# Performance work log

Hardware: AMD Instinct MI355X
Metric: run time of the kernel (lower is better)

## Reference

```python
import jax, jax.numpy as jnp
import numpy as np

B, N, INDIM, OUTDIM = 32, 128, 32, 64


def setup_inputs() -> dict:
    key = jax.random.key(0)
    k1, k2, k3, k4, k5, k6 = jax.random.split(key, 6)
    X = jax.random.normal(k1, (B, N, N, INDIM), dtype=jnp.float32)
    # variable subgraph sizes (irregular masking), at least 1 node per graph
    n_nodes = jnp.clip(jax.random.randint(k2, (B,), 0, N), 1, N).astype(jnp.int64)
    # MLP params (Linear + ReLU tail activation) for lin1 and lin2
    s = 1.0 / np.sqrt(INDIM)
    W1 = jax.random.uniform(k3, (INDIM, OUTDIM), jnp.float32, -s, s)
    b1 = jax.random.uniform(k4, (OUTDIM,), jnp.float32, -s, s)
    W2 = jax.random.uniform(k5, (INDIM, OUTDIM), jnp.float32, -s, s)
    b2 = jax.random.uniform(k6, (OUTDIM,), jnp.float32, -s, s)
    return {"X": X, "W1": W1, "b1": b1, "W2": W2, "b2": b2, "n_nodes": n_nodes}


def reference(X, W1, b1, W2, b2, n_nodes):
    # pairwise mask [B,N,N,1] from per-graph node counts (MaskedTensor mode 'DD')
    nm = jnp.arange(N)[None, :] < n_nodes[:, None]          # [B,N] node mask
    mask = (nm[:, :, None] & nm[:, None, :])[..., None].astype(X.dtype)  # [B,N,N,1]
    # tuplewiseapply of lin1 / lin2 (Linear + ReLU), zero-fill masked tuples
    X1 = jax.nn.relu(jnp.einsum('bijd,de->bije', X, W1) + b1) * mask  # [B,N,N,OUTDIM]
    X2 = jax.nn.relu(jnp.einsum('bijd,de->bije', X, W2) + b2) * mask
    # Op2FWL (aggr='sum'): per-channel batched matmul over node dim k
    out = jnp.einsum('bike,bkje->bije', X1, X2) * mask
    return out
```

## Files before the change

kernel.cpp:

```cpp
#include <hip/hip_runtime.h>

typedef unsigned short ushort_t;
typedef __attribute__((ext_vector_type(8))) __bf16 bf16x8;
typedef __attribute__((ext_vector_type(4))) float f32x4;


__device__ __forceinline__ ushort_t f32_to_bf16(float v) {
    unsigned ui = __float_as_uint(v);
    ui += 0x7fffu + ((ui >> 16) & 1u);
    return (ushort_t)(ui >> 16);
}

union FragU { bf16x8 f; ushort_t u[8]; };
union Pack4 { ushort_t us[4]; uint2 v; };

__global__ __launch_bounds__(256) void lin_mfma_kernel(
        const float* __restrict__ X,
        const float* __restrict__ W1, const float* __restrict__ b1v,
        const float* __restrict__ W2, const float* __restrict__ b2v,
        const int* __restrict__ n_nodes,
        ushort_t* __restrict__ X1t, ushort_t* __restrict__ X2t) {
    __shared__ ushort_t sO[64 * 136];
    const int blk = blockIdx.x;
    const int pass = blk >> 10;
    const int idx = blk & 1023;
    const int b = idx >> 5, rg = idx & 31;
    const float* W    = pass ? W2  : W1;
    const float* bias = pass ? b2v : b1v;
    ushort_t* Out     = pass ? X2t : X1t;
    const int rstride = pass ? 32 : 4096;
    const int tstride = pass ? 4096 : 32;

    const int u = threadIdx.x;
    const int w = u >> 6, l = u & 63;
    const int quad = l >> 4, lid = l & 15;
    const int n = n_nodes[b];

    FragU bfrag[4];
    float bia[4];
    #pragma unroll
    for (int ni = 0; ni < 4; ++ni) {
        const int e = ni * 16 + lid;
        #pragma unroll
        for (int j = 0; j < 8; ++j)
            bfrag[ni].u[j] = f32_to_bf16(W[(quad * 8 + j) * 64 + e]);
        bia[ni] = bias[e];
    }

    for (int q = 0; q < 4; ++q) {
        const int r = rg * 4 + q;
        const bool rin = (r < n);
        if (rin) {
            const float* Xb = X + (size_t)b * 524288 + (size_t)r * rstride;
            #pragma unroll
            for (int s = 0; s < 2; ++s) {
                const int mt = w * 2 + s;
                const int t0b = mt * 16 + quad * 4;
                if (mt * 16 < n) {
                    const int m = mt * 16 + lid;
                    const float* xr = Xb + (size_t)m * tstride + quad * 8;
                    float4 x0 = *(const float4*)xr;
                    float4 x1 = *(const float4*)(xr + 4);
                    FragU af;
                    af.u[0] = f32_to_bf16(x0.x); af.u[1] = f32_to_bf16(x0.y);
                    af.u[2] = f32_to_bf16(x0.z); af.u[3] = f32_to_bf16(x0.w);
                    af.u[4] = f32_to_bf16(x1.x); af.u[5] = f32_to_bf16(x1.y);
                    af.u[6] = f32_to_bf16(x1.z); af.u[7] = f32_to_bf16(x1.w);
                    #pragma unroll
                    for (int ni = 0; ni < 4; ++ni) {
                        f32x4 acc = {};
                        acc = __builtin_amdgcn_mfma_f32_16x16x32_bf16(
                            af.f, bfrag[ni].f, acc, 0, 0, 0);
                        const int e = ni * 16 + lid;
                        Pack4 pk;
                        #pragma unroll
                        for (int rgi = 0; rgi < 4; ++rgi) {
                            const int t = t0b + rgi;
                            float v = (t < n) ? fmaxf(acc[rgi] + bia[ni], 0.f) : 0.f;
                            pk.us[rgi] = f32_to_bf16(v);
                        }
                        *(uint2*)(sO + e * 136 + t0b) = pk.v;
                    }
                } else {
                    Pack4 pk; pk.us[0] = pk.us[1] = pk.us[2] = pk.us[3] = 0;
                    #pragma unroll
                    for (int ni = 0; ni < 4; ++ni)
                        *(uint2*)(sO + (ni * 16 + lid) * 136 + t0b) = pk.v;
                }
            }
        }
        __syncthreads();
        {
            const int e = u >> 2, part = u & 3;
            ushort_t* gO = Out + ((size_t)(b * 64 + e) * 128 + r) * 128 + part * 32;
            if (rin) {
                const ushort_t* sRow = sO + e * 136 + part * 32;
                #pragma unroll
                for (int c = 0; c < 4; ++c)
                    *(uint4*)(gO + c * 8) = *(const uint4*)(sRow + c * 8);
            } else {
                uint4 z = {0, 0, 0, 0};
                #pragma unroll
                for (int c = 0; c < 4; ++c)
                    *(uint4*)(gO + c * 8) = z;
            }
        }
        __syncthreads();
    }
}

__global__ __launch_bounds__(256) void mm_kernel(
        const ushort_t* __restrict__ X1t, const ushort_t* __restrict__ X2t,
        ushort_t* __restrict__ Ct, const int* __restrict__ n_nodes) {
    __shared__ ushort_t sC[128 * 136];
    const int blk = blockIdx.x;
    const size_t plane = (size_t)blk * 16384;
    const int n = n_nodes[blk >> 6];
    const int kmax = (n + 31) & ~31;
    const ushort_t* Aj = X2t + plane;
    const ushort_t* Bi = X1t + plane;
    const int u = threadIdx.x;
    const int w = u >> 6, l = u & 63;
    const int quad = l >> 4, lid = l & 15;
    const int wj = (w >> 1) * 64, wi = (w & 1) * 64;
    const bool anyA = (wj < n), anyB = (wi < n);
    bool aAct[4], bAct[4];
    #pragma unroll
    for (int mj = 0; mj < 4; ++mj) aAct[mj] = (wj + mj * 16) < n;
    #pragma unroll
    for (int ni = 0; ni < 4; ++ni) bAct[ni] = (wi + ni * 16) < n;
    f32x4 acc[4][4] = {};

    for (int k0 = 0; k0 < kmax; k0 += 32) {
        bf16x8 af[4], bfr[4];
        #pragma unroll
        for (int mj = 0; mj < 4; ++mj)
            if (aAct[mj] && anyB)
                af[mj] = *(const bf16x8*)(Aj + (size_t)(wj + mj * 16 + lid) * 128 + k0 + quad * 8);
        #pragma unroll
        for (int ni = 0; ni < 4; ++ni)
            if (bAct[ni] && anyA)
                bfr[ni] = *(const bf16x8*)(Bi + (size_t)(wi + ni * 16 + lid) * 128 + k0 + quad * 8);
        #pragma unroll
        for (int mj = 0; mj < 4; ++mj)
            #pragma unroll
            for (int ni = 0; ni < 4; ++ni)
                if (aAct[mj] && bAct[ni])
                    acc[mj][ni] = __builtin_amdgcn_mfma_f32_16x16x32_bf16(
                        af[mj], bfr[ni], acc[mj][ni], 0, 0, 0);
    }

    #pragma unroll
    for (int mj = 0; mj < 4; ++mj)
        #pragma unroll
        for (int ni = 0; ni < 4; ++ni) {
            const int j0 = wj + mj * 16 + quad * 4;
            const int i  = wi + ni * 16 + lid;
            Pack4 pk;
            #pragma unroll
            for (int rg = 0; rg < 4; ++rg)
                pk.us[rg] = f32_to_bf16(acc[mj][ni][rg]);
            *(uint2*)(sC + i * 136 + j0) = pk.v;
        }
    __syncthreads();
    ushort_t* Cp = Ct + plane;
    #pragma unroll
    for (int it = 0; it < 8; ++it) {
        int idx = it * 256 + u;
        int i = idx >> 4, c = idx & 15;
        *(uint4*)(Cp + (size_t)idx * 8) = *(const uint4*)(sC + i * 136 + c * 8);
    }
}

__global__ __launch_bounds__(256) void tr_kernel(
        const ushort_t* __restrict__ Ct, float* __restrict__ out,
        const int* __restrict__ n_nodes) {
    __shared__ float sT[64 * 129];
    const int blk = blockIdx.x;
    const int b = blk >> 7, i = blk & 127;
    const int u = threadIdx.x;
    const int n = n_nodes[b];
    float* ob = out + ((size_t)b * 16384 + (size_t)i * 128) * 64;

    if (i >= n) {
        float4 z = {0.f, 0.f, 0.f, 0.f};
        #pragma unroll
        for (int it = 0; it < 8; ++it)
            *(float4*)(ob + (size_t)(it * 256 + u) * 4) = z;
        return;
    }

    const ushort_t* Cb = Ct + (size_t)b * 1048576 + (size_t)i * 128;
    #pragma unroll
    for (int it = 0; it < 4; ++it) {
        int idx = it * 256 + u;
        int e = idx >> 4, c = idx & 15;
        float* dst = sT + e * 129 + c * 8;
        if (c * 8 < n) {
            uint4 v = *(const uint4*)(Cb + (size_t)e * 16384 + c * 8);
            dst[0] = __uint_as_float(v.x << 16);
            dst[1] = __uint_as_float(v.x & 0xffff0000u);
            dst[2] = __uint_as_float(v.y << 16);
            dst[3] = __uint_as_float(v.y & 0xffff0000u);
            dst[4] = __uint_as_float(v.z << 16);
            dst[5] = __uint_as_float(v.z & 0xffff0000u);
            dst[6] = __uint_as_float(v.w << 16);
            dst[7] = __uint_as_float(v.w & 0xffff0000u);
        } else {
            #pragma unroll
            for (int t = 0; t < 8; ++t) dst[t] = 0.f;
        }
    }
    __syncthreads();

    #pragma unroll
    for (int it = 0; it < 8; ++it) {
        int idx = it * 256 + u;
        int j = idx >> 4, e0 = (idx & 15) * 4;
        float4 vv;
        vv.x = sT[(e0 + 0) * 129 + j];
        vv.y = sT[(e0 + 1) * 129 + j];
        vv.z = sT[(e0 + 2) * 129 + j];
        vv.w = sT[(e0 + 3) * 129 + j];
        *(float4*)(ob + (size_t)idx * 4) = vv;
    }
}

extern "C" void kernel_launch(void* const* d_in, const int* in_sizes, int n_in,
                              void* d_out, int out_size, void* d_ws, size_t ws_size,
                              hipStream_t stream) {
    const float* X  = (const float*)d_in[0];
    const float* W1 = (const float*)d_in[1];
    const float* b1 = (const float*)d_in[2];
    const float* W2 = (const float*)d_in[3];
    const float* b2 = (const float*)d_in[4];
    const int* nn   = (const int*)d_in[5];
    float* out = (float*)d_out;

    ushort_t* X1t = (ushort_t*)d_ws;
    ushort_t* X2t = X1t + 33554432;
    ushort_t* Ct  = X1t;

    lin_mfma_kernel<<<2048, 256, 0, stream>>>(X, W1, b1, W2, b2, nn, X1t, X2t);
    mm_kernel<<<2048, 256, 0, stream>>>(X1t, X2t, Ct, nn);
    tr_kernel<<<4096, 256, 0, stream>>>(Ct, out, nn);
}
```

Measured before the change: 270.8 us.

## Fuse channel matmul with output transpose and skip masked rows in linear stage

Replaces the separate bf16 batched-matmul and transpose kernels with one kernel. Each block computes a 32x32 (i,j) tile for all 64 channels, stages the results in shared memory, and writes fp32 output directly in [b,i,j,e] layout, so the intermediate bf16 C plane no longer goes to global memory and back. Fully masked tiles only write zeros. The linear kernel now exits early for row groups past n and skips zero-filling out-of-range rows and column parts, which saves global writes. In exchange the new grid is only 512 blocks with a serial loop over channel groups, which lowers parallelism, and some masked-out rows are read uninitialized and then discarded by selects.

```diff
diff --git a/kernel.cpp b/kernel.cpp
--- a/kernel.cpp
+++ b/kernel.cpp
@@ -25,6 +25,9 @@
     const int pass = blk >> 10;
     const int idx = blk & 1023;
     const int b = idx >> 5, rg = idx & 31;
+    const int n = n_nodes[b];
+    if (rg * 4 >= n) return;
+
     const float* W    = pass ? W2  : W1;
     const float* bias = pass ? b2v : b1v;
     ushort_t* Out     = pass ? X2t : X1t;
@@ -34,7 +37,6 @@
     const int u = threadIdx.x;
     const int w = u >> 6, l = u & 63;
     const int quad = l >> 4, lid = l & 15;
-    const int n = n_nodes[b];
 
     FragU bfrag[4];
     float bia[4];
@@ -49,8 +51,8 @@
 
     for (int q = 0; q < 4; ++q) {
         const int r = rg * 4 + q;
-        const bool rin = (r < n);
-        if (rin) {
+        if (r >= n) break;
+        {
             const float* Xb = X + (size_t)b * 524288 + (size_t)r * rstride;
             #pragma unroll
             for (int s = 0; s < 2; ++s) {
@@ -92,137 +94,110 @@
         __syncthreads();
         {
             const int e = u >> 2, part = u & 3;
-            ushort_t* gO = Out + ((size_t)(b * 64 + e) * 128 + r) * 128 + part * 32;
-            if (rin) {
+            if (part * 32 < n) {
+                ushort_t* gO = Out + ((size_t)(b * 64 + e) * 128 + r) * 128 + part * 32;
                 const ushort_t* sRow = sO + e * 136 + part * 32;
                 #pragma unroll
                 for (int c = 0; c < 4; ++c)
                     *(uint4*)(gO + c * 8) = *(const uint4*)(sRow + c * 8);
-            } else {
-                uint4 z = {0, 0, 0, 0};
-                #pragma unroll
-                for (int c = 0; c < 4; ++c)
-                    *(uint4*)(gO + c * 8) = z;
-            }
-        }
-        __syncthreads();
-    }
-}
-
-__global__ __launch_bounds__(256) void mm_kernel(
+            }
+        }
+        __syncthreads();
+    }
+}
+
+__global__ __launch_bounds__(256) void mmtr_kernel(
         const ushort_t* __restrict__ X1t, const ushort_t* __restrict__ X2t,
-        ushort_t* __restrict__ Ct, const int* __restrict__ n_nodes) {
-    __shared__ ushort_t sC[128 * 136];
+        float* __restrict__ out, const int* __restrict__ n_nodes) {
+    __shared__ float sC[8 * 32 * 36];
     const int blk = blockIdx.x;
-    const size_t plane = (size_t)blk * 16384;
-    const int n = n_nodes[blk >> 6];
-    const int kmax = (n + 31) & ~31;
-    const ushort_t* Aj = X2t + plane;
-    const ushort_t* Bi = X1t + plane;
+    const int b = blk >> 4, it = (blk >> 2) & 3, jt = blk & 3;
+    const int i0 = it * 32, j0 = jt * 32;
+    const int n = n_nodes[b];
     const int u = threadIdx.x;
+    float* base = out + ((size_t)((b * 128 + i0) * 128 + j0)) * 64;
+
+    if (i0 >= n || j0 >= n) {
+        float4 z = {0.f, 0.f, 0.f, 0.f};
+        for (int il = 0; il < 32; ++il) {
+            float4* r = (float4*)(base + (size_t)il * 8192);
+            r[u] = z; r[u + 256] = z;
+        }
+        return;
+    }
+
     const int w = u >> 6, l = u & 63;
     const int quad = l >> 4, lid = l & 15;
-    const int wj = (w >> 1) * 64, wi = (w & 1) * 64;
-    const bool anyA = (wj < n), anyB = (wi < n);
-    bool aAct[4], bAct[4];
-    #pragma unroll
-    for (int mj = 0; mj < 4; ++mj) aAct[mj] = (wj + mj * 16) < n;
-    #pragma unroll
-    for (int ni = 0; ni < 4; ++ni) bAct[ni] = (wi + ni * 16) < n;
-    f32x4 acc[4][4] = {};
-
-    for (int k0 = 0; k0 < kmax; k0 += 32) {
-        bf16x8 af[4], bfr[4];
+    const int kmax = (n + 31) & ~31;
+    const size_t pb = (size_t)(b * 64) * 16384;
+    const ushort_t* Aj = X2t + pb;
+    const ushort_t* Bi = X1t + pb;
+
+    for (int g = 0; g < 8; ++g) {
+        const int e0 = g * 8 + w * 2;
+        const ushort_t* A0 = Aj + (size_t)e0 * 16384;
+        const ushort_t* B0 = Bi + (size_t)e0 * 16384;
+        const ushort_t* A1 = A0 + 16384;
+        const ushort_t* B1 = B0 + 16384;
+        f32x4 acc[2][2][2] = {};
+
+        for (int k0 = 0; k0 < kmax; k0 += 32) {
+            bf16x8 a0[2], a1[2], b0[2], b1[2];
+            #pragma unroll
+            for (int mj = 0; mj < 2; ++mj) {
+                const size_t off = (size_t)(j0 + mj * 16 + lid) * 128 + k0 + quad * 8;
+                a0[mj] = *(const bf16x8*)(A0 + off);
+                a1[mj] = *(const bf16x8*)(A1 + off);
+            }
+            #pragma unroll
+            for (int ni = 0; ni < 2; ++ni) {
+                const size_t off = (size_t)(i0 + ni * 16 + lid) * 128 + k0 + quad * 8;
+                b0[ni] = *(const bf16x8*)(B0 + off);
+                b1[ni] = *(const bf16x8*)(B1 + off);
+            }
+            #pragma unroll
+            for (int mj = 0; mj < 2; ++mj)
+                #pragma unroll
+                for (int ni = 0; ni < 2; ++ni) {
+                    acc[0][mj][ni] = __builtin_amdgcn_mfma_f32_16x16x32_bf16(
+                        a0[mj], b0[ni], acc[0][mj][ni], 0, 0, 0);
+                    acc[1][mj][ni] = __builtin_amdgcn_mfma_f32_16x16x32_bf16(
+                        a1[mj], b1[ni], acc[1][mj][ni], 0, 0, 0);
+                }
+        }
+
         #pragma unroll
-        for (int mj = 0; mj < 4; ++mj)
-            if (aAct[mj] && anyB)
-                af[mj] = *(const bf16x8*)(Aj + (size_t)(wj + mj * 16 + lid) * 128 + k0 + quad * 8);
+        for (int ee = 0; ee < 2; ++ee) {
+            const int el = w * 2 + ee;
+            #pragma unroll
+            for (int mj = 0; mj < 2; ++mj)
+                #pragma unroll
+                for (int ni = 0; ni < 2; ++ni) {
+                    const int il = ni * 16 + lid;
+                    const int jl = mj * 16 + quad * 4;
+                    const bool iin = (i0 + il) < n;
+                    float4 v;
+                    v.x = (iin && (j0 + jl + 0) < n) ? acc[ee][mj][ni][0] : 0.f;
+                    v.y = (iin && (j0 + jl + 1) < n) ? acc[ee][mj][ni][1] : 0.f;
+                    v.z = (iin && (j0 + jl + 2) < n) ? acc[ee][mj][ni][2] : 0.f;
+                    v.w = (iin && (j0 + jl + 3) < n) ? acc[ee][mj][ni][3] : 0.f;
+                    *(float4*)(&sC[(el * 32 + il) * 36 + jl]) = v;
+                }
+        }
+        __syncthreads();
+
         #pragma unroll
-        for (int ni = 0; ni < 4; ++ni)
-            if (bAct[ni] && anyA)
-                bfr[ni] = *(const bf16x8*)(Bi + (size_t)(wi + ni * 16 + lid) * 128 + k0 + quad * 8);
-        #pragma unroll
-        for (int mj = 0; mj < 4; ++mj)
-            #pragma unroll
-            for (int ni = 0; ni < 4; ++ni)
-                if (aAct[mj] && bAct[ni])
-                    acc[mj][ni] = __builtin_amdgcn_mfma_f32_16x16x32_bf16(
-                        af[mj], bfr[ni], acc[mj][ni], 0, 0, 0);
-    }
-
-    #pragma unroll
-    for (int mj = 0; mj < 4; ++mj)
-        #pragma unroll
-        for (int ni = 0; ni < 4; ++ni) {
-            const int j0 = wj + mj * 16 + quad * 4;
-            const int i  = wi + ni * 16 + lid;
-            Pack4 pk;
-            #pragma unroll
-            for (int rg = 0; rg < 4; ++rg)
-                pk.us[rg] = f32_to_bf16(acc[mj][ni][rg]);
-            *(uint2*)(sC + i * 136 + j0) = pk.v;
-        }
-    __syncthreads();
-    ushort_t* Cp = Ct + plane;
-    #pragma unroll
-    for (int it = 0; it < 8; ++it) {
-        int idx = it * 256 + u;
-        int i = idx >> 4, c = idx & 15;
-        *(uint4*)(Cp + (size_t)idx * 8) = *(const uint4*)(sC + i * 136 + c * 8);
-    }
-}
-
-__global__ __launch_bounds__(256) void tr_kernel(
-        const ushort_t* __restrict__ Ct, float* __restrict__ out,
-        const int* __restrict__ n_nodes) {
-    __shared__ float sT[64 * 129];
-    const int blk = blockIdx.x;
-    const int b = blk >> 7, i = blk & 127;
-    const int u = threadIdx.x;
-    const int n = n_nodes[b];
-    float* ob = out + ((size_t)b * 16384 + (size_t)i * 128) * 64;
-
-    if (i >= n) {
-        float4 z = {0.f, 0.f, 0.f, 0.f};
-        #pragma unroll
-        for (int it = 0; it < 8; ++it)
-            *(float4*)(ob + (size_t)(it * 256 + u) * 4) = z;
-        return;
-    }
-
-    const ushort_t* Cb = Ct + (size_t)b * 1048576 + (size_t)i * 128;
-    #pragma unroll
-    for (int it = 0; it < 4; ++it) {
-        int idx = it * 256 + u;
-        int e = idx >> 4, c = idx & 15;
-        float* dst = sT + e * 129 + c * 8;
-        if (c * 8 < n) {
-            uint4 v = *(const uint4*)(Cb + (size_t)e * 16384 + c * 8);
-            dst[0] = __uint_as_float(v.x << 16);
-            dst[1] = __uint_as_float(v.x & 0xffff0000u);
-            dst[2] = __uint_as_float(v.y << 16);
-            dst[3] = __uint_as_float(v.y & 0xffff0000u);
-            dst[4] = __uint_as_float(v.z << 16);
-            dst[5] = __uint_as_float(v.z & 0xffff0000u);
-            dst[6] = __uint_as_float(v.w << 16);
-            dst[7] = __uint_as_float(v.w & 0xffff0000u);
-        } else {
-            #pragma unroll
-            for (int t = 0; t < 8; ++t) dst[t] = 0.f;
-        }
-    }
-    __syncthreads();
-
-    #pragma unroll
-    for (int it = 0; it < 8; ++it) {
-        int idx = it * 256 + u;
-        int j = idx >> 4, e0 = (idx & 15) * 4;
-        float4 vv;
-        vv.x = sT[(e0 + 0) * 129 + j];
-        vv.y = sT[(e0 + 1) * 129 + j];
-        vv.z = sT[(e0 + 2) * 129 + j];
-        vv.w = sT[(e0 + 3) * 129 + j];
-        *(float4*)(ob + (size_t)idx * 4) = vv;
+        for (int rep = 0; rep < 8; ++rep) {
+            const int idx = rep * 256 + u;
+            const int elq = idx & 1, jl = (idx >> 1) & 31, il = idx >> 6;
+            float4 vv;
+            vv.x = sC[((elq * 4 + 0) * 32 + il) * 36 + jl];
+            vv.y = sC[((elq * 4 + 1) * 32 + il) * 36 + jl];
+            vv.z = sC[((elq * 4 + 2) * 32 + il) * 36 + jl];
+            vv.w = sC[((elq * 4 + 3) * 32 + il) * 36 + jl];
+            *(float4*)(base + (size_t)il * 8192 + jl * 64 + g * 8 + elq * 4) = vv;
+        }
+        __syncthreads();
     }
 }
 
@@ -239,9 +214,7 @@
 
     ushort_t* X1t = (ushort_t*)d_ws;
     ushort_t* X2t = X1t + 33554432;
-    ushort_t* Ct  = X1t;
 
     lin_mfma_kernel<<<2048, 256, 0, stream>>>(X, W1, b1, W2, b2, nn, X1t, X2t);
-    mm_kernel<<<2048, 256, 0, stream>>>(X1t, X2t, Ct, nn);
-    tr_kernel<<<4096, 256, 0, stream>>>(Ct, out, nn);
-}
+    mmtr_kernel<<<512, 256, 0, stream>>>(X1t, X2t, out, nn);
+}
```

New measurement: 317.5 us. 17.2% more time.
